# Kernel optimization log

Hardware: AMD Instinct MI355X
Metric: run time of the kernel (lower is better)

## Reference

```python
import jax, jax.numpy as jnp
import numpy as np
from itertools import combinations

DIM = 7
EPS = 1e-4

# --- static exterior-derivative index maps (mirrors _build_derivative_maps d2_map) ---
_IDX3 = list(combinations(range(DIM), 3))           # 35 ordered 3-form multi-indices
_POS2 = {t: i for i, t in enumerate(combinations(range(DIM), 2))}  # 21 2-form positions
_d2 = []
for _out, (i, j, k) in enumerate(_IDX3):
    for _p, (a, b, c) in enumerate([(i, j, k), (j, i, k), (k, i, j)]):
        bc = tuple(sorted((b, c)))
        s = (-1) ** _p * (1 if (b, c) == bc else -1)
        _d2.append((_out, _POS2[bc], a, s))
OUT_POS = np.array([t[0] for t in _d2], dtype=np.int32)   # (105,)
IN_POS  = np.array([t[1] for t in _d2], dtype=np.int32)   # (105,)
DCOORD  = np.array([t[2] for t in _d2], dtype=np.int32)   # (105,)
SIGNS   = np.array([t[3] for t in _d2], dtype=np.float32) # (105,)


def setup_inputs() -> dict:
    key = jax.random.key(0)
    k1, k2, k3 = jax.random.split(key, 3)
    B = 262144
    x = jax.random.normal(k1, (B, DIM), dtype=jnp.float32)
    W1 = jax.random.normal(k2, (DIM, 32), dtype=jnp.float32) * 0.3
    W2 = jax.random.normal(k3, (32, 21), dtype=jnp.float32) * 0.3
    return {"x": x, "W1": W1, "W2": W2}


def reference(x, W1, W2):
    """ExteriorDerivative.apply_2form_fd with omega_fn(x) = sin(x @ W1) @ W2.

    x: (B, 7) -> d_omega: (B, 35)
    """
    def omega_fn(xx):  # (..., 7) -> (..., 21)
        return jnp.sin(xx @ W1) @ W2

    B = x.shape[0]
    # All 7 +/- coordinate perturbations at once: (7, B, 7)
    pert = EPS * jnp.eye(DIM, dtype=x.dtype)[:, None, :]
    omega_plus = omega_fn(x[None] + pert)    # (7, B, 21)
    omega_minus = omega_fn(x[None] - pert)   # (7, B, 21)
    fd = (omega_plus - omega_minus) / (2.0 * EPS)  # central differences (7, B, 21)

    # Gather the 105 (deriv_coord, in_pos) derivative values -> (105, B)
    grads = fd[DCOORD, :, IN_POS]
    contrib = jnp.asarray(SIGNS)[:, None] * grads  # (105, B)

    # Scatter-add into the 35 3-form components (duplicate out positions accumulate)
    d_omega = jnp.zeros((B, 35), dtype=x.dtype).at[:, OUT_POS].add(contrib.T)
    return d_omega
```

## Files before the change

### kernel.cpp

```cpp
#include <hip/hip_runtime.h>

#define DIM 7
#define HD  32
#define P2  21
#define P3  35
#define BLK 256
#define NT  3
#define TPW 4
#define WPB (BLK / 64)
#define WSLAB (TPW * 16 * DIM)

typedef __attribute__((ext_vector_type(8))) _Float16 half8v;
typedef __attribute__((ext_vector_type(4))) float  float4v;

static __device__ const int TI[P3] = {
  0,0,0,0,0,0,0,0,0,0,0,0,0,0,0,
  1,1,1,1,1,1,1,1,1,1,
  2,2,2,2,2,2,
  3,3,3,
  4};
static __device__ const int TJ[P3] = {
  1,1,1,1,1, 2,2,2,2, 3,3,3, 4,4, 5,
  2,2,2,2, 3,3,3, 4,4, 5,
  3,3,3, 4,4, 5,
  4,4, 5,
  5};
static __device__ const int TK[P3] = {
  2,3,4,5,6, 3,4,5,6, 4,5,6, 5,6, 6,
  3,4,5,6, 4,5,6, 5,6, 6,
  4,5,6, 5,6, 6,
  5,6, 6,
  6};

__device__ __forceinline__ int pos2(int a, int b) {
  return a * 6 - (a * (a - 1)) / 2 + (b - a - 1);
}

__global__ __launch_bounds__(BLK)
void dform_kernel(const float* __restrict__ x,
                  const float* __restrict__ W1,
                  const float* __restrict__ W2,
                  float* __restrict__ out, int B)
{
  __shared__ _Float16 Mh[NT * 16 * HD];
  __shared__ float xs[WPB * WSLAB];

  const int tid  = threadIdx.x;
  const int lane = tid & 63;
  const int wid  = tid >> 6;
  const int lrow = lane & 15;
  const int lgrp = lane >> 4;

  for (int idx = tid; idx < NT * 16 * HD; idx += BLK) {
    int col = idx >> 5;
    int h   = idx & (HD - 1);
    float val = 0.f;
    if (col < P3) {
      int i = TI[col], j = TJ[col], k = TK[col];
      val = W1[i * HD + h] * W2[h * P2 + pos2(j, k)]
          - W1[j * HD + h] * W2[h * P2 + pos2(i, k)]
          + W1[k * HD + h] * W2[h * P2 + pos2(i, j)];
    }
    Mh[idx] = (_Float16)val;
  }

  const int h0 = lgrp * 8;
  float w1r[DIM][8];
  #pragma unroll
  for (int j = 0; j < DIM; ++j) {
    float4 p0 = *reinterpret_cast<const float4*>(&W1[j * HD + h0]);
    float4 p1 = *reinterpret_cast<const float4*>(&W1[j * HD + h0 + 4]);
    w1r[j][0] = p0.x; w1r[j][1] = p0.y; w1r[j][2] = p0.z; w1r[j][3] = p0.w;
    w1r[j][4] = p1.x; w1r[j][5] = p1.y; w1r[j][6] = p1.z; w1r[j][7] = p1.w;
  }

  const int gw = blockIdx.x * WPB + wid;
  const int tb = gw * TPW;
  const long long xbase = (long long)gw * WSLAB;
  float* xw = xs + wid * WSLAB;
  if (xbase + WSLAB <= (long long)B * DIM) {
    const float4* src = reinterpret_cast<const float4*>(x + xbase);
    float4* dst = reinterpret_cast<float4*>(xw);
    dst[lane] = src[lane];
    if (lane < WSLAB / 4 - 64) dst[lane + 64] = src[lane + 64];
  } else {
    for (int i = lane; i < WSLAB; i += 64) {
      long long g = xbase + i;
      xw[i] = (g < (long long)B * DIM) ? x[g] : 0.f;
    }
  }

  __syncthreads();

  half8v mfrag[NT];
  #pragma unroll
  for (int c = 0; c < NT; ++c) {
    int off = (c * 16 + lrow) * HD + h0;
    mfrag[c] = *reinterpret_cast<const half8v*>(&Mh[off]);
  }

  float xr[TPW][DIM];
  #pragma unroll
  for (int i = 0; i < TPW; ++i)
    #pragma unroll
    for (int j = 0; j < DIM; ++j)
      xr[i][j] = xw[(i * 16 + lrow) * DIM + j];

  #pragma unroll
  for (int i = 0; i < TPW; ++i) {
    const int t = tb + i;
    if (t * 16 >= B) break;

    half8v cfrag;
    #pragma unroll
    for (int e = 0; e < 8; ++e) {
      float tv = 0.f;
      #pragma unroll
      for (int j = 0; j < DIM; ++j) tv = fmaf(xr[i][j], w1r[j][e], tv);
      cfrag[e] = (_Float16)__cosf(tv);
    }

    float4v acc[NT];
    #pragma unroll
    for (int c = 0; c < NT; ++c) {
      acc[c][0] = 0.f; acc[c][1] = 0.f; acc[c][2] = 0.f; acc[c][3] = 0.f;
      acc[c] = __builtin_amdgcn_mfma_f32_16x16x32_f16(mfrag[c], cfrag, acc[c], 0, 0, 0);
    }

    const int row = t * 16 + lrow;
    if (row < B) {
      float* op = out + (long long)row * P3;
      const int cb = lgrp * 4;
      *reinterpret_cast<float4*>(op + cb) =
          make_float4(acc[0][0], acc[0][1], acc[0][2], acc[0][3]);
      *reinterpret_cast<float4*>(op + 16 + cb) =
          make_float4(acc[1][0], acc[1][1], acc[1][2], acc[1][3]);
      if (lgrp == 0) {
        *reinterpret_cast<float2*>(op + 32) = make_float2(acc[2][0], acc[2][1]);
        op[34] = acc[2][2];
      }
    }
  }
}

extern "C" void kernel_launch(void* const* d_in, const int* in_sizes, int n_in,
                              void* d_out, int out_size, void* d_ws, size_t ws_size,
                              hipStream_t stream) {
  const float* x  = (const float*)d_in[0];
  const float* W1 = (const float*)d_in[1];
  const float* W2 = (const float*)d_in[2];
  float* out = (float*)d_out;
  const int B = in_sizes[0] / DIM;
  const int ntiles = (B + 15) / 16;
  const int waves  = (ntiles + TPW - 1) / TPW;
  const int grid   = (waves + WPB - 1) / WPB;
  hipLaunchKernelGGL(dform_kernel, dim3(grid), dim3(BLK), 0, stream,
                     x, W1, W2, out, B);
}
```

Before: 19.49 us.

## Stage weights in LDS, pad M tile, halve tiles per wave, use nontemporal stores

Copies W1 and W2 into shared memory once per block and builds the fused M matrix from LDS, using packed triple indices and a padded stride to cut bank conflicts. The cosine fragments for all tiles are computed up front, W1 is read from LDS instead of being held in registers, and tiles per wave drop from 4 to 2 to launch more waves. Output stores become nontemporal to avoid cache pollution. Fewer tiles per wave means the per-block setup of M runs over less useful work, and an extra barrier is added.

```diff
diff --git a/kernel.cpp b/kernel.cpp
--- a/kernel.cpp
+++ b/kernel.cpp
@@ -6,83 +6,75 @@
 #define P3  35
 #define BLK 256
 #define NT  3
-#define TPW 4
+#define TPW 2
 #define WPB (BLK / 64)
 #define WSLAB (TPW * 16 * DIM)
+#define MSTR 40
 
 typedef __attribute__((ext_vector_type(8))) _Float16 half8v;
 typedef __attribute__((ext_vector_type(4))) float  float4v;
+typedef __attribute__((ext_vector_type(2))) float  float2v;
 
-static __device__ const int TI[P3] = {
-  0,0,0,0,0,0,0,0,0,0,0,0,0,0,0,
-  1,1,1,1,1,1,1,1,1,1,
-  2,2,2,2,2,2,
-  3,3,3,
-  4};
-static __device__ const int TJ[P3] = {
-  1,1,1,1,1, 2,2,2,2, 3,3,3, 4,4, 5,
-  2,2,2,2, 3,3,3, 4,4, 5,
-  3,3,3, 4,4, 5,
-  4,4, 5,
-  5};
-static __device__ const int TK[P3] = {
-  2,3,4,5,6, 3,4,5,6, 4,5,6, 5,6, 6,
-  3,4,5,6, 4,5,6, 5,6, 6,
-  4,5,6, 5,6, 6,
-  5,6, 6,
-  6};
+static __device__ const unsigned TRIP[P3] = {
+  0x020100,0x030100,0x040100,0x050100,0x060100,
+  0x030200,0x040200,0x050200,0x060200,
+  0x040300,0x050300,0x060300,
+  0x050400,0x060400,
+  0x060500,
+  0x030201,0x040201,0x050201,0x060201,
+  0x040301,0x050301,0x060301,
+  0x050401,0x060401,
+  0x060501,
+  0x040302,0x050302,0x060302,
+  0x050402,0x060402,
+  0x060502,
+  0x050403,0x060403,
+  0x060503,
+  0x060504};
 
 __device__ __forceinline__ int pos2(int a, int b) {
   return a * 6 - (a * (a - 1)) / 2 + (b - a - 1);
 }
 
-__global__ __launch_bounds__(BLK)
+__device__ __forceinline__ void nts4(float* p, float4v v) {
+  __builtin_nontemporal_store(v, reinterpret_cast<float4v*>(p));
+}
+__device__ __forceinline__ void nts2(float* p, float2v v) {
+  __builtin_nontemporal_store(v, reinterpret_cast<float2v*>(p));
+}
+__device__ __forceinline__ void nts1(float* p, float v) {
+  __builtin_nontemporal_store(v, p);
+}
+
+__global__ __launch_bounds__(BLK, 6)
 void dform_kernel(const float* __restrict__ x,
                   const float* __restrict__ W1,
                   const float* __restrict__ W2,
                   float* __restrict__ out, int B)
 {
-  __shared__ _Float16 Mh[NT * 16 * HD];
-  __shared__ float xs[WPB * WSLAB];
+  __shared__ float    sW1[DIM][HD + 1];
+  __shared__ float    sW2[HD * P2];
+  __shared__ _Float16 Mh[NT * 16 * MSTR];
+  __shared__ float    xs[WPB][WSLAB];
 
   const int tid  = threadIdx.x;
   const int lane = tid & 63;
   const int wid  = tid >> 6;
   const int lrow = lane & 15;
   const int lgrp = lane >> 4;
+  const int h0   = lgrp * 8;
 
-  for (int idx = tid; idx < NT * 16 * HD; idx += BLK) {
-    int col = idx >> 5;
-    int h   = idx & (HD - 1);
-    float val = 0.f;
-    if (col < P3) {
-      int i = TI[col], j = TJ[col], k = TK[col];
-      val = W1[i * HD + h] * W2[h * P2 + pos2(j, k)]
-          - W1[j * HD + h] * W2[h * P2 + pos2(i, k)]
-          + W1[k * HD + h] * W2[h * P2 + pos2(i, j)];
-    }
-    Mh[idx] = (_Float16)val;
-  }
-
-  const int h0 = lgrp * 8;
-  float w1r[DIM][8];
-  #pragma unroll
-  for (int j = 0; j < DIM; ++j) {
-    float4 p0 = *reinterpret_cast<const float4*>(&W1[j * HD + h0]);
-    float4 p1 = *reinterpret_cast<const float4*>(&W1[j * HD + h0 + 4]);
-    w1r[j][0] = p0.x; w1r[j][1] = p0.y; w1r[j][2] = p0.z; w1r[j][3] = p0.w;
-    w1r[j][4] = p1.x; w1r[j][5] = p1.y; w1r[j][6] = p1.z; w1r[j][7] = p1.w;
-  }
+  for (int idx = tid; idx < DIM * HD; idx += BLK) sW1[idx / HD][idx % HD] = W1[idx];
+  for (int idx = tid; idx < HD * P2; idx += BLK) sW2[idx] = W2[idx];
 
   const int gw = blockIdx.x * WPB + wid;
   const int tb = gw * TPW;
   const long long xbase = (long long)gw * WSLAB;
-  float* xw = xs + wid * WSLAB;
+  float* xw = &xs[wid][0];
   if (xbase + WSLAB <= (long long)B * DIM) {
-    const float4* src = reinterpret_cast<const float4*>(x + xbase);
-    float4* dst = reinterpret_cast<float4*>(xw);
-    dst[lane] = src[lane];
-    if (lane < WSLAB / 4 - 64) dst[lane + 64] = src[lane + 64];
+    const float4v* src = reinterpret_cast<const float4v*>(x + xbase);
+    float4v* dst = reinterpret_cast<float4v*>(xw);
+    if (lane < WSLAB / 4) dst[lane] = src[lane];
   } else {
     for (int i = lane; i < WSLAB; i += 64) {
       long long g = xbase + i;
@@ -92,12 +84,19 @@
 
   __syncthreads();
 
-  half8v mfrag[NT];
-  #pragma unroll
-  for (int c = 0; c < NT; ++c) {
-    int off = (c * 16 + lrow) * HD + h0;
-    mfrag[c] = *reinterpret_cast<const half8v*>(&Mh[off]);
+  for (int idx = tid; idx < NT * 16 * HD; idx += BLK) {
+    int col = idx >> 5, h = idx & (HD - 1);
+    float val = 0.f;
+    if (col < P3) {
+      unsigned tr = TRIP[col];
+      int i = tr & 255, j = (tr >> 8) & 255, k = (tr >> 16) & 255;
+      val = sW1[i][h] * sW2[h * P2 + pos2(j, k)]
+          - sW1[j][h] * sW2[h * P2 + pos2(i, k)]
+          + sW1[k][h] * sW2[h * P2 + pos2(i, j)];
+    }
+    Mh[col * MSTR + h] = (_Float16)val;
   }
+  __syncthreads();
 
   float xr[TPW][DIM];
   #pragma unroll
@@ -106,38 +105,47 @@
     for (int j = 0; j < DIM; ++j)
       xr[i][j] = xw[(i * 16 + lrow) * DIM + j];
 
+  half8v cf[TPW];
+  #pragma unroll
+  for (int e = 0; e < 8; ++e) {
+    float w[DIM];
+    #pragma unroll
+    for (int j = 0; j < DIM; ++j) w[j] = sW1[j][h0 + e];
+    #pragma unroll
+    for (int i = 0; i < TPW; ++i) {
+      float tv = 0.f;
+      #pragma unroll
+      for (int j = 0; j < DIM; ++j) tv = fmaf(xr[i][j], w[j], tv);
+      cf[i][e] = (_Float16)__cosf(tv);
+    }
+  }
+
+  half8v mfrag[NT];
+  #pragma unroll
+  for (int c = 0; c < NT; ++c)
+    mfrag[c] = *reinterpret_cast<const half8v*>(&Mh[(c * 16 + lrow) * MSTR + h0]);
+
   #pragma unroll
   for (int i = 0; i < TPW; ++i) {
     const int t = tb + i;
     if (t * 16 >= B) break;
 
-    half8v cfrag;
-    #pragma unroll
-    for (int e = 0; e < 8; ++e) {
-      float tv = 0.f;
-      #pragma unroll
-      for (int j = 0; j < DIM; ++j) tv = fmaf(xr[i][j], w1r[j][e], tv);
-      cfrag[e] = (_Float16)__cosf(tv);
-    }
-
     float4v acc[NT];
     #pragma unroll
     for (int c = 0; c < NT; ++c) {
-      acc[c][0] = 0.f; acc[c][1] = 0.f; acc[c][2] = 0.f; acc[c][3] = 0.f;
-      acc[c] = __builtin_amdgcn_mfma_f32_16x16x32_f16(mfrag[c], cfrag, acc[c], 0, 0, 0);
+      acc[c] = (float4v){0.f, 0.f, 0.f, 0.f};
+      acc[c] = __builtin_amdgcn_mfma_f32_16x16x32_f16(mfrag[c], cf[i], acc[c], 0, 0, 0);
     }
 
     const int row = t * 16 + lrow;
     if (row < B) {
       float* op = out + (long long)row * P3;
       const int cb = lgrp * 4;
-      *reinterpret_cast<float4*>(op + cb) =
-          make_float4(acc[0][0], acc[0][1], acc[0][2], acc[0][3]);
-      *reinterpret_cast<float4*>(op + 16 + cb) =
-          make_float4(acc[1][0], acc[1][1], acc[1][2], acc[1][3]);
+      nts4(op + cb,      acc[0]);
+      nts4(op + 16 + cb, acc[1]);
       if (lgrp == 0) {
-        *reinterpret_cast<float2*>(op + 32) = make_float2(acc[2][0], acc[2][1]);
-        op[34] = acc[2][2];
+        nts2(op + 32, (float2v){acc[2][0], acc[2][1]});
+        nts1(op + 34, acc[2][2]);
       }
     }
   }
```

Measured after the change: 31.33 us. 1.61x slower.
